# Performance work log

Measured on AMD Instinct MI355X. Metric: run time of the kernel, lower is better.

Reference implementation:

```python
import jax, jax.numpy as jnp
import numpy as np

N = 50000
E = 800000
IN, HID, OUT = 256, 128, 64
NEG_SLOPE = 0.2


def _gat(x, src, dst, W, a_src, a_dst, b, heads, dim, concat):
    # PyG GATConv (eval mode, self-loops already appended to src/dst)
    xh = (x @ W).reshape(N, heads, dim)              # [N,H,D]
    s_src = jnp.einsum('nhd,hd->nh', xh, a_src)       # [N,H]
    s_dst = jnp.einsum('nhd,hd->nh', xh, a_dst)
    e = jax.nn.leaky_relu(s_src[src] + s_dst[dst], NEG_SLOPE)  # [Etot,H]
    m = jax.ops.segment_max(e, dst, num_segments=N)
    e = jnp.exp(e - m[dst])
    z = jax.ops.segment_sum(e, dst, num_segments=N)
    alpha = e / z[dst]                                # segment softmax over incoming edges
    msg = xh[src] * alpha[:, :, None]                 # [Etot,H,D] gather + weight
    out = jax.ops.segment_sum(msg, dst, num_segments=N)  # scatter-add aggregate
    out = out.reshape(N, heads * dim) if concat else out.mean(axis=1)
    return out + b


def setup_inputs():
    key = jax.random.key(0)
    ks = jax.random.split(key, 20)
    sc = 0.05
    inp = {
        'x': jax.random.normal(ks[0], (N, IN), jnp.float32),
        'edge_index': jax.random.randint(ks[1], (2, E), 0, N, jnp.int64) if jax.config.read('jax_enable_x64') else jax.random.randint(ks[1], (2, E), 0, N, jnp.int32),
        # semantic MLP
        'w1': jax.random.normal(ks[2], (IN, HID), jnp.float32) * sc,
        'b1': jnp.zeros((HID,), jnp.float32),
        'w2': jax.random.normal(ks[3], (HID, HID), jnp.float32) * sc,
        'b2': jnp.zeros((HID,), jnp.float32),
        # gat1: HID -> HID//2, heads=4, concat -> 2*HID
        'g1_w': jax.random.normal(ks[4], (HID, 4 * (HID // 2)), jnp.float32) * sc,
        'g1_asrc': jax.random.normal(ks[5], (4, HID // 2), jnp.float32) * sc,
        'g1_adst': jax.random.normal(ks[6], (4, HID // 2), jnp.float32) * sc,
        'g1_b': jnp.zeros((2 * HID,), jnp.float32),
        # gat2: 2*HID -> OUT, heads=2, mean
        'g2_w': jax.random.normal(ks[7], (2 * HID, 2 * OUT), jnp.float32) * sc,
        'g2_asrc': jax.random.normal(ks[8], (2, OUT), jnp.float32) * sc,
        'g2_adst': jax.random.normal(ks[9], (2, OUT), jnp.float32) * sc,
        'g2_b': jnp.zeros((OUT,), jnp.float32),
        # gat3: OUT -> OUT, heads=1, mean
        'g3_w': jax.random.normal(ks[10], (OUT, OUT), jnp.float32) * sc,
        'g3_asrc': jax.random.normal(ks[11], (1, OUT), jnp.float32) * sc,
        'g3_adst': jax.random.normal(ks[12], (1, OUT), jnp.float32) * sc,
        'g3_b': jnp.zeros((OUT,), jnp.float32),
    }
    return inp


def reference(x, edge_index, w1, b1, w2, b2,
              g1_w, g1_asrc, g1_adst, g1_b,
              g2_w, g2_asrc, g2_adst, g2_b,
              g3_w, g3_asrc, g3_adst, g3_b):
    # add self loops once (PyG GATConv default add_self_loops=True)
    loop = jnp.arange(N, dtype=edge_index.dtype)
    src = jnp.concatenate([edge_index[0], loop])
    dst = jnp.concatenate([edge_index[1], loop])
    # semantic MLP (eval: dropout is identity)
    h = jax.nn.relu(x @ w1 + b1)
    h = jax.nn.relu(h @ w2 + b2)
    h = jax.nn.elu(_gat(h, src, dst, g1_w, g1_asrc, g1_adst, g1_b, 4, HID // 2, True))
    h = jax.nn.elu(_gat(h, src, dst, g2_w, g2_asrc, g2_adst, g2_b, 2, OUT, False))
    h = _gat(h, src, dst, g3_w, g3_asrc, g3_adst, g3_b, 1, OUT, False)
    return h
```

## Files before the change

kernel.cpp:

```cpp
#include <hip/hip_runtime.h>
#include <hip/hip_fp16.h>
#include <math.h>

#define NN 50000
#define NE 800000

static inline int ceil_div_h(int a, int b) { return (a + b - 1) / b; }

typedef _Float16 half8 __attribute__((ext_vector_type(8)));
typedef float f32x4 __attribute__((ext_vector_type(4)));

__global__ __launch_bounds__(256)
void prep_kernel(const float* __restrict__ w1, const float* __restrict__ w2,
                 const float* __restrict__ g1w, const float* __restrict__ g2w,
                 const float* __restrict__ g3w, __half* __restrict__ wt,
                 int* __restrict__ cursor) {
  int idx = blockIdx.x * 256 + threadIdx.x;
  if (idx < NN) cursor[idx] = 0;
  const float* W; int K, N, li;
  if (idx < 32768)        { W = w1;  K = 256; N = 128; li = idx; }
  else if (idx < 49152)   { W = w2;  K = 128; N = 128; li = idx - 32768; }
  else if (idx < 81920)   { W = g1w; K = 128; N = 256; li = idx - 49152; }
  else if (idx < 114688)  { W = g2w; K = 256; N = 128; li = idx - 81920; }
  else if (idx < 118784)  { W = g3w; K = 64;  N = 64;  li = idx - 114688; }
  else return;
  int n = li / K, k = li - n * K;
  wt[idx] = __float2half_rn(W[(size_t)k * N + n]);
}

__global__ __launch_bounds__(256)
void mlp_gat1_fused(const float* __restrict__ x,
                    const __half* __restrict__ wt1,
                    const float* __restrict__ b1,
                    const __half* __restrict__ wt2,
                    const float* __restrict__ b2,
                    const __half* __restrict__ wtg1,
                    const float* __restrict__ a_src, const float* __restrict__ a_dst,
                    __half* __restrict__ xh1,
                    float* __restrict__ s_src, float* __restrict__ s_dst) {
  constexpr int SA = 40;
  constexpr int SH = 136;
  __shared__ __align__(16) _Float16 smem[25088];
  _Float16* As   = smem;
  _Float16* Bs12 = smem + 2560;
  _Float16* h1s  = smem + 7680;
  _Float16* h2s  = smem + 16384;
  _Float16* Bs3  = Bs12;
  const int tid = threadIdx.x;
  const int bm = blockIdx.x * 64;
  const int wave = tid >> 6, lane = tid & 63;
  const int l16 = lane & 15, quad = lane >> 4;
  const int wm = (wave & 1) * 32;
  const int wn = (wave >> 1) * 64;

  {
    f32x4 acc[2][4] = {};
    for (int k0 = 0; k0 < 256; k0 += 32) {
      #pragma unroll
      for (int i = 0; i < 2; ++i) {
        int idx = tid + i * 256;
        int m = idx >> 3, q = idx & 7;
        int gm = bm + m;
        float4 v = make_float4(0.f, 0.f, 0.f, 0.f);
        if (gm < NN) v = *(const float4*)&x[(size_t)gm * 256 + k0 + q * 4];
        union { __half2 h2[2]; float2 f2; } u;
        u.h2[0] = __floats2half2_rn(v.x, v.y);
        u.h2[1] = __floats2half2_rn(v.z, v.w);
        *(float2*)&As[m * SA + q * 4] = u.f2;
      }
      #pragma unroll
      for (int i = 0; i < 2; ++i) {
        int idx = tid + i * 256;
        int n = idx >> 2, kq = (idx & 3) * 8;
        *(float4*)&Bs12[n * SA + kq] = *(const float4*)&wt1[(size_t)n * 256 + k0 + kq];
      }
      __syncthreads();
      half8 af[2], bf[4];
      #pragma unroll
      for (int mi = 0; mi < 2; ++mi)
        af[mi] = *(const half8*)&As[(wm + mi * 16 + l16) * SA + quad * 8];
      #pragma unroll
      for (int ni = 0; ni < 4; ++ni)
        bf[ni] = *(const half8*)&Bs12[(wn + ni * 16 + l16) * SA + quad * 8];
      #pragma unroll
      for (int mi = 0; mi < 2; ++mi)
        #pragma unroll
        for (int ni = 0; ni < 4; ++ni)
          acc[mi][ni] = __builtin_amdgcn_mfma_f32_16x16x32_f16(af[mi], bf[ni], acc[mi][ni], 0, 0, 0);
      __syncthreads();
    }
    #pragma unroll
    for (int mi = 0; mi < 2; ++mi)
      #pragma unroll
      for (int r = 0; r < 4; ++r) {
        int row = wm + mi * 16 + quad * 4 + r;
        #pragma unroll
        for (int ni = 0; ni < 4; ++ni) {
          int col = wn + ni * 16 + l16;
          float v = acc[mi][ni][r] + b1[col];
          v = fmaxf(v, 0.f);
          h1s[row * SH + col] = (_Float16)v;
        }
      }
  }
  __syncthreads();

  {
    f32x4 acc[2][4] = {};
    for (int k0 = 0; k0 < 128; k0 += 32) {
      #pragma unroll
      for (int i = 0; i < 2; ++i) {
        int idx = tid + i * 256;
        int n = idx >> 2, kq = (idx & 3) * 8;
        *(float4*)&Bs12[n * SA + kq] = *(const float4*)&wt2[(size_t)n * 128 + k0 + kq];
      }
      __syncthreads();
      half8 af[2], bf[4];
      #pragma unroll
      for (int mi = 0; mi < 2; ++mi)
        af[mi] = *(const half8*)&h1s[(wm + mi * 16 + l16) * SH + k0 + quad * 8];
      #pragma unroll
      for (int ni = 0; ni < 4; ++ni)
        bf[ni] = *(const half8*)&Bs12[(wn + ni * 16 + l16) * SA + quad * 8];
      #pragma unroll
      for (int mi = 0; mi < 2; ++mi)
        #pragma unroll
        for (int ni = 0; ni < 4; ++ni)
          acc[mi][ni] = __builtin_amdgcn_mfma_f32_16x16x32_f16(af[mi], bf[ni], acc[mi][ni], 0, 0, 0);
      __syncthreads();
    }
    #pragma unroll
    for (int mi = 0; mi < 2; ++mi)
      #pragma unroll
      for (int r = 0; r < 4; ++r) {
        int row = wm + mi * 16 + quad * 4 + r;
        #pragma unroll
        for (int ni = 0; ni < 4; ++ni) {
          int col = wn + ni * 16 + l16;
          float v = acc[mi][ni][r] + b2[col];
          v = fmaxf(v, 0.f);
          h2s[row * SH + col] = (_Float16)v;
        }
      }
  }
  __syncthreads();

  {
    f32x4 acc[4][4] = {};
    const int wn3 = wave * 64;
    for (int k0 = 0; k0 < 128; k0 += 32) {
      #pragma unroll
      for (int i = 0; i < 4; ++i) {
        int idx = tid + i * 256;
        int n = idx >> 2, kq = (idx & 3) * 8;
        *(float4*)&Bs3[n * SA + kq] = *(const float4*)&wtg1[(size_t)n * 128 + k0 + kq];
      }
      __syncthreads();
      half8 af[4], bf[4];
      #pragma unroll
      for (int mi = 0; mi < 4; ++mi)
        af[mi] = *(const half8*)&h2s[(mi * 16 + l16) * SH + k0 + quad * 8];
      #pragma unroll
      for (int ni = 0; ni < 4; ++ni)
        bf[ni] = *(const half8*)&Bs3[(wn3 + ni * 16 + l16) * SA + quad * 8];
      #pragma unroll
      for (int mi = 0; mi < 4; ++mi)
        #pragma unroll
        for (int ni = 0; ni < 4; ++ni)
          acc[mi][ni] = __builtin_amdgcn_mfma_f32_16x16x32_f16(af[mi], bf[ni], acc[mi][ni], 0, 0, 0);
      __syncthreads();
    }
    float asv[4], adv[4];
    #pragma unroll
    for (int ni = 0; ni < 4; ++ni) {
      int d = ni * 16 + l16;
      asv[ni] = a_src[wave * 64 + d];
      adv[ni] = a_dst[wave * 64 + d];
    }
    #pragma unroll
    for (int mi = 0; mi < 4; ++mi) {
      #pragma unroll
      for (int r = 0; r < 4; ++r) {
        int gm = bm + mi * 16 + quad * 4 + r;
        float ss = 0.f, sd = 0.f;
        #pragma unroll
        for (int ni = 0; ni < 4; ++ni) {
          float v = acc[mi][ni][r];
          ss = fmaf(v, asv[ni], ss);
          sd = fmaf(v, adv[ni], sd);
          if (gm < NN) xh1[(size_t)gm * 256 + wn3 + ni * 16 + l16] = __float2half_rn(v);
        }
        #pragma unroll
        for (int off = 1; off < 16; off <<= 1) {
          ss += __shfl_xor(ss, off, 64);
          sd += __shfl_xor(sd, off, 64);
        }
        if (l16 == 0 && gm < NN) {
          s_src[gm * 4 + wave] = ss;
          s_dst[gm * 4 + wave] = sd;
        }
      }
    }
  }
}

template<int BM, int TN, int WR, int WC, int ACT, int OUTH, int AF32, int HS>
__global__ __launch_bounds__(256)
void mfma_gemm(const void* __restrict__ Av, const __half* __restrict__ Bt,
               const float* __restrict__ bias, void* __restrict__ Cv,
               const float* __restrict__ a_src, const float* __restrict__ a_dst,
               float* __restrict__ s_src, float* __restrict__ s_dst,
               int M, int N, int K) {
  constexpr int FM = BM / WR / 16;
  constexpr int FN = TN / WC / 16;
  constexpr int SA = 40;
  __shared__ __align__(16) _Float16 As[BM * SA];
  __shared__ __align__(16) _Float16 Bs[TN * SA];
  const int tid = threadIdx.x;
  const int bm = blockIdx.y * BM, bn = blockIdx.x * TN;
  const int wave = tid >> 6, lane = tid & 63;
  const int wm = (wave % WR) * (BM / WR);
  const int wn = (wave / WR) * (TN / WC);
  const int l16 = lane & 15, quad = lane >> 4;

  f32x4 acc[FM][FN] = {};

  for (int k0 = 0; k0 < K; k0 += 32) {
    if (AF32) {
      const float* A = (const float*)Av;
      #pragma unroll
      for (int i = 0; i < (BM * 8) / 256; ++i) {
        int idx = tid + i * 256;
        int m = idx >> 3, q = idx & 7;
        int gm = bm + m;
        float4 v = make_float4(0.f, 0.f, 0.f, 0.f);
        if (gm < M) v = *(const float4*)&A[(size_t)gm * K + k0 + q * 4];
        union { __half2 h2[2]; float2 f2; } u;
        u.h2[0] = __floats2half2_rn(v.x, v.y);
        u.h2[1] = __floats2half2_rn(v.z, v.w);
        *(float2*)&As[m * SA + q * 4] = u.f2;
      }
    } else {
      const __half* A = (const __half*)Av;
      #pragma unroll
      for (int i = 0; i < (BM * 4) / 256; ++i) {
        int idx = tid + i * 256;
        int m = idx >> 2, q = (idx & 3) * 8;
        int gm = bm + m;
        float4 raw = make_float4(0.f, 0.f, 0.f, 0.f);
        if (gm < M) raw = *(const float4*)&A[(size_t)gm * K + k0 + q];
        *(float4*)&As[m * SA + q] = raw;
      }
    }
    #pragma unroll
    for (int i = 0; i < (TN * 4) / 256; ++i) {
      int idx = tid + i * 256;
      int n = idx >> 2, kq = (idx & 3) * 8;
      float4 raw = *(const float4*)&Bt[(size_t)(bn + n) * K + k0 + kq];
      *(float4*)&Bs[n * SA + kq] = raw;
    }
    __syncthreads();
    half8 af[FM], bf[FN];
    #pragma unroll
    for (int mi = 0; mi < FM; ++mi)
      af[mi] = *(const half8*)&As[(wm + mi * 16 + l16) * SA + quad * 8];
    #pragma unroll
    for (int ni = 0; ni < FN; ++ni)
      bf[ni] = *(const half8*)&Bs[(wn + ni * 16 + l16) * SA + quad * 8];
    #pragma unroll
    for (int mi = 0; mi < FM; ++mi)
      #pragma unroll
      for (int ni = 0; ni < FN; ++ni)
        acc[mi][ni] = __builtin_amdgcn_mfma_f32_16x16x32_f16(af[mi], bf[ni], acc[mi][ni], 0, 0, 0);
    __syncthreads();
  }

  #pragma unroll
  for (int mi = 0; mi < FM; ++mi) {
    #pragma unroll
    for (int r = 0; r < 4; ++r) {
      int gm = bm + wm + mi * 16 + quad * 4 + r;
      if (gm >= M) continue;
      #pragma unroll
      for (int ni = 0; ni < FN; ++ni) {
        int gn = bn + wn + ni * 16 + l16;
        float v = acc[mi][ni][r];
        if (bias) v += bias[gn];
        if (ACT == 1) v = fmaxf(v, 0.f);
        if (OUTH) ((__half*)Cv)[(size_t)gm * N + gn] = __float2half_rn(v);
        else      ((float*)Cv)[(size_t)gm * N + gn] = v;
      }
    }
  }

  if (HS > 0) {
    const int h = (bn + wn) >> 6;
    float asv[FN], adv[FN];
    #pragma unroll
    for (int ni = 0; ni < FN; ++ni) {
      int d = ni * 16 + l16;
      asv[ni] = a_src[h * 64 + d];
      adv[ni] = a_dst[h * 64 + d];
    }
    #pragma unroll
    for (int mi = 0; mi < FM; ++mi) {
      #pragma unroll
      for (int r = 0; r < 4; ++r) {
        float ss = 0.f, sd = 0.f;
        #pragma unroll
        for (int ni = 0; ni < FN; ++ni) {
          float v = acc[mi][ni][r];
          ss = fmaf(v, asv[ni], ss);
          sd = fmaf(v, adv[ni], sd);
        }
        #pragma unroll
        for (int off = 1; off < 16; off <<= 1) {
          ss += __shfl_xor(ss, off, 64);
          sd += __shfl_xor(sd, off, 64);
        }
        int gm = bm + wm + mi * 16 + quad * 4 + r;
        if (l16 == 0 && gm < M) {
          s_src[gm * HS + h] = ss;
          s_dst[gm * HS + h] = sd;
        }
      }
    }
  }
}


__global__ __launch_bounds__(256)
void hist_kernel(const int* __restrict__ ei, int* __restrict__ cnt) {
  int e = blockIdx.x * blockDim.x + threadIdx.x;
  if (e >= NE) return;
  atomicAdd(&cnt[ei[NE + e]], 1);
}

__global__ __launch_bounds__(256)
void scan1_kernel(const int* __restrict__ in, int* __restrict__ out,
                  int* __restrict__ bsum, int n) {
  __shared__ int tmp[256];
  int t = threadIdx.x;
  int i = blockIdx.x * 256 + t;
  int v = (i < n) ? in[i] : 0;
  tmp[t] = v;
  __syncthreads();
  for (int off = 1; off < 256; off <<= 1) {
    int u = (t >= off) ? tmp[t - off] : 0;
    __syncthreads();
    tmp[t] += u;
    __syncthreads();
  }
  if (i <= n) out[i] = tmp[t] - v;
  if (t == 255) bsum[blockIdx.x] = tmp[255];
}

__global__ __launch_bounds__(256)
void scan3_kernel(int* __restrict__ out, const int* __restrict__ bsum,
                  int* __restrict__ cursor, int n, int nb) {
  __shared__ int tmp[256];
  int t = threadIdx.x;
  int bv = (t < nb) ? bsum[t] : 0;
  tmp[t] = bv;
  __syncthreads();
  for (int off = 1; off < 256; off <<= 1) {
    int u = (t >= off) ? tmp[t - off] : 0;
    __syncthreads();
    tmp[t] += u;
    __syncthreads();
  }
  int add = tmp[blockIdx.x] - ((blockIdx.x < nb) ? bsum[blockIdx.x] : 0);
  int i = blockIdx.x * 256 + t;
  if (i > n) return;
  int v = out[i] + add;
  out[i] = v;
  if (i < n) cursor[i] = v;
}

__global__ __launch_bounds__(256)
void scatter_kernel(const int* __restrict__ ei, int* __restrict__ cursor,
                    int* __restrict__ srcs) {
  int e = blockIdx.x * blockDim.x + threadIdx.x;
  if (e >= NE) return;
  int s = ei[e], d = ei[NE + e];
  int pos = atomicAdd(&cursor[d], 1);
  srcs[pos] = s;
}

__global__ __launch_bounds__(256)
void gat_aggregate4(const int* __restrict__ rowptr, const int* __restrict__ srcs,
                    const float* __restrict__ ssrc, const float* __restrict__ sdst,
                    const __half* __restrict__ xh, const float* __restrict__ bias,
                    __half* __restrict__ out) {
  constexpr int H = 4, HD = 256;
  __shared__ float wbuf[4][64 * H];
  __shared__ int sbuf[4][64];
  const int wslot = threadIdx.x >> 6;
  const int wid = (blockIdx.x * blockDim.x + threadIdx.x) >> 6;
  const int lane = threadIdx.x & 63;
  if (wid >= NN) return;
  const int n = wid;
  const int start = rowptr[n];
  const int end = rowptr[n + 1];
  const int h = lane >> 4;

  float sdv[H];
  #pragma unroll
  for (int hh = 0; hh < H; ++hh) sdv[hh] = sdst[n * H + hh];

  float z;
  float acc[H];
  {
    float wself[H];
    #pragma unroll
    for (int hh = 0; hh < H; ++hh) {
      float e = ssrc[n * H + hh] + sdv[hh];
      e = e >= 0.f ? e : 0.2f * e;
      wself[hh] = __expf(e);
    }
    float ws = wself[h];
    z = ws;
    const __half* xr = xh + (size_t)n * HD + lane * H;
    float2 raw = *(const float2*)xr;
    __half2 p0 = *(__half2*)&raw.x;
    __half2 p1 = *(__half2*)&raw.y;
    float2 f0 = __half22float2(p0), f1 = __half22float2(p1);
    acc[0] = ws * f0.x; acc[1] = ws * f0.y; acc[2] = ws * f1.x; acc[3] = ws * f1.y;
  }

  for (int base = start; base < end; base += 64) {
    int cnt = end - base;
    if (cnt > 64) cnt = 64;
    if (lane < cnt) {
      int s = srcs[base + lane];
      sbuf[wslot][lane] = s;
      float4 t = *(const float4*)&ssrc[s * 4];
      float ev[H] = {t.x, t.y, t.z, t.w};
      #pragma unroll
      for (int hh = 0; hh < H; ++hh) {
        float e = ev[hh] + sdv[hh];
        e = e >= 0.f ? e : 0.2f * e;
        wbuf[wslot][lane * H + hh] = __expf(e);
      }
    }
    #pragma unroll 4
    for (int j = 0; j < cnt; ++j) {
      int s = sbuf[wslot][j];
      float w = wbuf[wslot][j * H + h];
      z += w;
      const __half* xr = xh + (size_t)s * HD + lane * H;
      float2 raw = *(const float2*)xr;
      __half2 p0 = *(__half2*)&raw.x;
      __half2 p1 = *(__half2*)&raw.y;
      float2 f0 = __half22float2(p0), f1 = __half22float2(p1);
      acc[0] = fmaf(w, f0.x, acc[0]); acc[1] = fmaf(w, f0.y, acc[1]);
      acc[2] = fmaf(w, f1.x, acc[2]); acc[3] = fmaf(w, f1.y, acc[3]);
    }
  }
  const float inv = 1.f / z;

  float v[4];
  #pragma unroll
  for (int i = 0; i < 4; ++i) {
    v[i] = acc[i] * inv + bias[lane * 4 + i];
    v[i] = v[i] > 0.f ? v[i] : expm1f(v[i]);
  }
  union { __half2 h2[2]; float2 f2; } u;
  u.h2[0] = __floats2half2_rn(v[0], v[1]);
  u.h2[1] = __floats2half2_rn(v[2], v[3]);
  *(float2*)&out[(size_t)n * 256 + lane * 4] = u.f2;
}

template<int H, int MODE>
__global__ __launch_bounds__(256)
void gat_aggregate_sub(const int* __restrict__ rowptr, const int* __restrict__ srcs,
                       const float* __restrict__ ssrc, const float* __restrict__ sdst,
                       const __half* __restrict__ xh, const float* __restrict__ bias,
                       void* __restrict__ outv) {
  constexpr int HD   = H * 64;
  constexpr int GL   = HD / 4;
  constexpr int NSUB = 64 / GL;
  const int wid  = (blockIdx.x * blockDim.x + threadIdx.x) >> 6;
  const int lane = threadIdx.x & 63;
  const int sg = lane / GL;
  const int p  = lane - sg * GL;
  const int n  = wid * NSUB + sg;
  const int hp = (p * 4) >> 6;
  const bool alive = (n < NN);

  int start = 0, end = 0;
  float sdv = 0.f;
  if (alive) {
    start = rowptr[n];
    end = rowptr[n + 1];
    sdv = sdst[n * H + hp];
  }

  float z = 0.f;
  float a0 = 0.f, a1 = 0.f, a2 = 0.f, a3 = 0.f;

  if (alive) {
    float e = ssrc[n * H + hp] + sdv;
    e = e >= 0.f ? e : 0.2f * e;
    float w = __expf(e);
    z = w;
    float2 raw = *(const float2*)(xh + (size_t)n * HD + p * 4);
    __half2 p0 = *(__half2*)&raw.x, p1 = *(__half2*)&raw.y;
    float2 f0 = __half22float2(p0), f1 = __half22float2(p1);
    a0 = w * f0.x; a1 = w * f0.y; a2 = w * f1.x; a3 = w * f1.y;
  }

  for (int j = start; j < end; ++j) {
    int s = srcs[j];
    float e = ssrc[s * H + hp] + sdv;
    e = e >= 0.f ? e : 0.2f * e;
    float w = __expf(e);
    z += w;
    float2 raw = *(const float2*)(xh + (size_t)s * HD + p * 4);
    __half2 p0 = *(__half2*)&raw.x, p1 = *(__half2*)&raw.y;
    float2 f0 = __half22float2(p0), f1 = __half22float2(p1);
    a0 = fmaf(w, f0.x, a0); a1 = fmaf(w, f0.y, a1);
    a2 = fmaf(w, f1.x, a2); a3 = fmaf(w, f1.y, a3);
  }

  const float inv = 1.f / z;

  if (MODE == 1) {
    float v0 = a0 * inv, v1 = a1 * inv, v2 = a2 * inv, v3 = a3 * inv;
    float o0 = __shfl_xor(v0, 16, 64);
    float o1 = __shfl_xor(v1, 16, 64);
    float o2 = __shfl_xor(v2, 16, 64);
    float o3 = __shfl_xor(v3, 16, 64);
    if (alive && hp == 0) {
      float m0 = (v0 + o0) * 0.5f + bias[p * 4 + 0];
      float m1 = (v1 + o1) * 0.5f + bias[p * 4 + 1];
      float m2 = (v2 + o2) * 0.5f + bias[p * 4 + 2];
      float m3 = (v3 + o3) * 0.5f + bias[p * 4 + 3];
      m0 = m0 > 0.f ? m0 : expm1f(m0);
      m1 = m1 > 0.f ? m1 : expm1f(m1);
      m2 = m2 > 0.f ? m2 : expm1f(m2);
      m3 = m3 > 0.f ? m3 : expm1f(m3);
      __half* out = (__half*)outv;
      union { __half2 h2[2]; float2 f2; } u;
      u.h2[0] = __floats2half2_rn(m0, m1);
      u.h2[1] = __floats2half2_rn(m2, m3);
      *(float2*)&out[(size_t)n * 64 + p * 4] = u.f2;
    }
  } else {
    if (alive) {
      float* out = (float*)outv;
      float4 o = make_float4(a0 * inv + bias[p * 4 + 0],
                             a1 * inv + bias[p * 4 + 1],
                             a2 * inv + bias[p * 4 + 2],
                             a3 * inv + bias[p * 4 + 3]);
      *(float4*)&out[(size_t)n * 64 + p * 4] = o;
    }
  }
}


extern "C" void kernel_launch(void* const* d_in, const int* in_sizes, int n_in,
                              void* d_out, int out_size, void* d_ws, size_t ws_size,
                              hipStream_t stream) {
  const float* x    = (const float*)d_in[0];
  const int*   ei   = (const int*)d_in[1];
  const float* w1   = (const float*)d_in[2];
  const float* b1   = (const float*)d_in[3];
  const float* w2   = (const float*)d_in[4];
  const float* b2   = (const float*)d_in[5];
  const float* g1w  = (const float*)d_in[6];
  const float* g1as = (const float*)d_in[7];
  const float* g1ad = (const float*)d_in[8];
  const float* g1b  = (const float*)d_in[9];
  const float* g2w  = (const float*)d_in[10];
  const float* g2as = (const float*)d_in[11];
  const float* g2ad = (const float*)d_in[12];
  const float* g2b  = (const float*)d_in[13];
  const float* g3w  = (const float*)d_in[14];
  const float* g3as = (const float*)d_in[15];
  const float* g3ad = (const float*)d_in[16];
  const float* g3b  = (const float*)d_in[17];
  float* out = (float*)d_out;

  float* ws   = (float*)d_ws;
  float* bufA = ws;
  float* bufB = bufA + (size_t)NN * 256;
  float* bufC = bufB + (size_t)NN * 256;
  float* ssrc = bufC + (size_t)NN * 256;
  float* sdst = ssrc + (size_t)NN * 4;
  int* rowptr = (int*)(sdst + (size_t)NN * 4);
  int* cursor = rowptr + (NN + 1);
  int* bsum   = cursor + NN;
  int* srcs   = bsum + 256;
  __half* wt   = (__half*)(srcs + NE);
  __half* wt1  = wt;
  __half* wt2  = wt + 32768;
  __half* wtg1 = wt + 49152;
  __half* wtg2 = wt + 81920;
  __half* wtg3 = wt + 114688;

  __half* xh1 = (__half*)bufC;
  __half* a1  = (__half*)bufA;
  __half* xh2 = (__half*)bufB;
  __half* a2  = (__half*)bufC;
  __half* xh3 = (__half*)bufB;

  const int TB = 256;
  const int grid_m = ceil_div_h(NN, 64);
  const int egrid = ceil_div_h(NE, TB);
  const int sgrid = ceil_div_h(NN + 1, TB);
  const int wgrid = ceil_div_h(NN, 4);

  prep_kernel<<<ceil_div_h(118784, TB), TB, 0, stream>>>(w1, w2, g1w, g2w, g3w, wt, cursor);

  hist_kernel<<<egrid, TB, 0, stream>>>(ei, cursor);
  scan1_kernel<<<sgrid, TB, 0, stream>>>(cursor, rowptr, bsum, NN);
  scan3_kernel<<<sgrid, TB, 0, stream>>>(rowptr, bsum, cursor, NN, sgrid);
  scatter_kernel<<<egrid, TB, 0, stream>>>(ei, cursor, srcs);

  mlp_gat1_fused<<<grid_m, TB, 0, stream>>>(x, wt1, b1, wt2, b2, wtg1,
                                            g1as, g1ad, xh1, ssrc, sdst);
  gat_aggregate4<<<wgrid, TB, 0, stream>>>(rowptr, srcs, ssrc, sdst, xh1, g1b, a1);

  mfma_gemm<64, 128, 2, 2, 0, 1, 0, 2><<<dim3(1, grid_m), TB, 0, stream>>>(
      a1, wtg2, nullptr, xh2, g2as, g2ad, ssrc, sdst, NN, 128, 256);
  gat_aggregate_sub<2, 1><<<ceil_div_h(NN, 8), TB, 0, stream>>>(
      rowptr, srcs, ssrc, sdst, xh2, g2b, a2);

  mfma_gemm<64, 64, 4, 1, 0, 1, 0, 1><<<dim3(1, grid_m), TB, 0, stream>>>(
      a2, wtg3, nullptr, xh3, g3as, g3ad, ssrc, sdst, NN, 64, 64);
  gat_aggregate_sub<1, 2><<<ceil_div_h(NN, 16), TB, 0, stream>>>(
      rowptr, srcs, ssrc, sdst, xh3, g3b, out);
}
```

Measured before the change: 431.0 us.

## Aggregate GAT layers 2/3 with one wavefront per node and edge sub-groups

Replaces the sub-wavefront-per-node aggregation for the second and third GAT layers with one wavefront per destination node. Lanes are split into sub-groups that process different incoming edges in parallel, and the partial sums are combined with xor shuffles at the end. Each 64-edge chunk has its attention weights and source indices computed once and staged in shared memory, so the exp is not recomputed per lane. This gives more memory-level parallelism per node, at the cost of launching more wavefronts and leaving lanes idle on low-degree nodes.

```diff
diff --git a/kernel.cpp b/kernel.cpp
--- a/kernel.cpp
+++ b/kernel.cpp
@@ -473,56 +473,92 @@
 
 template<int H, int MODE>
 __global__ __launch_bounds__(256)
-void gat_aggregate_sub(const int* __restrict__ rowptr, const int* __restrict__ srcs,
-                       const float* __restrict__ ssrc, const float* __restrict__ sdst,
-                       const __half* __restrict__ xh, const float* __restrict__ bias,
-                       void* __restrict__ outv) {
+void gat_aggregate_ms(const int* __restrict__ rowptr, const int* __restrict__ srcs,
+                      const float* __restrict__ ssrc, const float* __restrict__ sdst,
+                      const __half* __restrict__ xh, const float* __restrict__ bias,
+                      void* __restrict__ outv) {
   constexpr int HD   = H * 64;
-  constexpr int GL   = HD / 4;
-  constexpr int NSUB = 64 / GL;
-  const int wid  = (blockIdx.x * blockDim.x + threadIdx.x) >> 6;
+  constexpr int L8   = HD / 4;
+  constexpr int NSUB = 64 / L8;
+  __shared__ float wbuf[4][64 * H];
+  __shared__ int sbuf[4][64];
+  const int wslot = threadIdx.x >> 6;
+  const int wid = (blockIdx.x * blockDim.x + threadIdx.x) >> 6;
   const int lane = threadIdx.x & 63;
-  const int sg = lane / GL;
-  const int p  = lane - sg * GL;
-  const int n  = wid * NSUB + sg;
+  if (wid >= NN) return;
+  const int n = wid;
+  const int start = rowptr[n];
+  const int end = rowptr[n + 1];
+  const int sub = lane / L8;
+  const int p = lane - sub * L8;
   const int hp = (p * 4) >> 6;
-  const bool alive = (n < NN);
-
-  int start = 0, end = 0;
-  float sdv = 0.f;
-  if (alive) {
-    start = rowptr[n];
-    end = rowptr[n + 1];
-    sdv = sdst[n * H + hp];
-  }
+
+  float sdv[H];
+  #pragma unroll
+  for (int hh = 0; hh < H; ++hh) sdv[hh] = sdst[n * H + hh];
 
   float z = 0.f;
   float a0 = 0.f, a1 = 0.f, a2 = 0.f, a3 = 0.f;
-
-  if (alive) {
-    float e = ssrc[n * H + hp] + sdv;
+  {
+    float e = ssrc[n * H + hp] + sdv[hp];
     e = e >= 0.f ? e : 0.2f * e;
-    float w = __expf(e);
-    z = w;
-    float2 raw = *(const float2*)(xh + (size_t)n * HD + p * 4);
-    __half2 p0 = *(__half2*)&raw.x, p1 = *(__half2*)&raw.y;
-    float2 f0 = __half22float2(p0), f1 = __half22float2(p1);
-    a0 = w * f0.x; a1 = w * f0.y; a2 = w * f1.x; a3 = w * f1.y;
-  }
-
-  for (int j = start; j < end; ++j) {
-    int s = srcs[j];
-    float e = ssrc[s * H + hp] + sdv;
-    e = e >= 0.f ? e : 0.2f * e;
-    float w = __expf(e);
-    z += w;
-    float2 raw = *(const float2*)(xh + (size_t)s * HD + p * 4);
-    __half2 p0 = *(__half2*)&raw.x, p1 = *(__half2*)&raw.y;
-    float2 f0 = __half22float2(p0), f1 = __half22float2(p1);
-    a0 = fmaf(w, f0.x, a0); a1 = fmaf(w, f0.y, a1);
-    a2 = fmaf(w, f1.x, a2); a3 = fmaf(w, f1.y, a3);
-  }
-
+    float ws = __expf(e);
+    if (sub == 0) {
+      z = ws;
+      float2 raw = *(const float2*)(xh + (size_t)n * HD + p * 4);
+      __half2 q0 = *(__half2*)&raw.x, q1 = *(__half2*)&raw.y;
+      float2 f0 = __half22float2(q0), f1 = __half22float2(q1);
+      a0 = ws * f0.x; a1 = ws * f0.y; a2 = ws * f1.x; a3 = ws * f1.y;
+    }
+  }
+
+  for (int base = start; base < end; base += 64) {
+    int cnt = end - base;
+    if (cnt > 64) cnt = 64;
+    int cnt_pad = (cnt + NSUB - 1) & ~(NSUB - 1);
+    if (lane < cnt) {
+      int s = srcs[base + lane];
+      sbuf[wslot][lane] = s;
+      float ev[H];
+      if (H == 2) {
+        float2 t = *(const float2*)&ssrc[s * 2];
+        ev[0] = t.x; ev[1] = t.y;
+      } else {
+        ev[0] = ssrc[s];
+      }
+      #pragma unroll
+      for (int hh = 0; hh < H; ++hh) {
+        float e = ev[hh] + sdv[hh];
+        e = e >= 0.f ? e : 0.2f * e;
+        wbuf[wslot][lane * H + hh] = __expf(e);
+      }
+    } else if (lane < cnt_pad) {
+      sbuf[wslot][lane] = n;
+      #pragma unroll
+      for (int hh = 0; hh < H; ++hh) wbuf[wslot][lane * H + hh] = 0.f;
+    }
+    #pragma unroll 4
+    for (int j = 0; j < cnt; j += NSUB) {
+      int e = j + sub;
+      int s = sbuf[wslot][e];
+      float w = wbuf[wslot][e * H + hp];
+      z += w;
+      float2 raw = *(const float2*)(xh + (size_t)s * HD + p * 4);
+      __half2 q0 = *(__half2*)&raw.x, q1 = *(__half2*)&raw.y;
+      float2 f0 = __half22float2(q0), f1 = __half22float2(q1);
+      a0 = fmaf(w, f0.x, a0); a1 = fmaf(w, f0.y, a1);
+      a2 = fmaf(w, f1.x, a2); a3 = fmaf(w, f1.y, a3);
+    }
+  }
+
+  #pragma unroll
+  for (int m = L8; m < 64; m <<= 1) {
+    z += __shfl_xor(z, m, 64);
+    a0 += __shfl_xor(a0, m, 64);
+    a1 += __shfl_xor(a1, m, 64);
+    a2 += __shfl_xor(a2, m, 64);
+    a3 += __shfl_xor(a3, m, 64);
+  }
   const float inv = 1.f / z;
 
   if (MODE == 1) {
@@ -531,7 +567,7 @@
     float o1 = __shfl_xor(v1, 16, 64);
     float o2 = __shfl_xor(v2, 16, 64);
     float o3 = __shfl_xor(v3, 16, 64);
-    if (alive && hp == 0) {
+    if (sub == 0 && hp == 0) {
       float m0 = (v0 + o0) * 0.5f + bias[p * 4 + 0];
       float m1 = (v1 + o1) * 0.5f + bias[p * 4 + 1];
       float m2 = (v2 + o2) * 0.5f + bias[p * 4 + 2];
@@ -547,7 +583,7 @@
       *(float2*)&out[(size_t)n * 64 + p * 4] = u.f2;
     }
   } else {
-    if (alive) {
+    if (sub == 0) {
       float* out = (float*)outv;
       float4 o = make_float4(a0 * inv + bias[p * 4 + 0],
                              a1 * inv + bias[p * 4 + 1],
@@ -624,11 +660,11 @@
 
   mfma_gemm<64, 128, 2, 2, 0, 1, 0, 2><<<dim3(1, grid_m), TB, 0, stream>>>(
       a1, wtg2, nullptr, xh2, g2as, g2ad, ssrc, sdst, NN, 128, 256);
-  gat_aggregate_sub<2, 1><<<ceil_div_h(NN, 8), TB, 0, stream>>>(
+  gat_aggregate_ms<2, 1><<<wgrid, TB, 0, stream>>>(
       rowptr, srcs, ssrc, sdst, xh2, g2b, a2);
 
   mfma_gemm<64, 64, 4, 1, 0, 1, 0, 1><<<dim3(1, grid_m), TB, 0, stream>>>(
       a2, wtg3, nullptr, xh3, g3as, g3ad, ssrc, sdst, NN, 64, 64);
-  gat_aggregate_sub<1, 2><<<ceil_div_h(NN, 16), TB, 0, stream>>>(
+  gat_aggregate_ms<1, 2><<<wgrid, TB, 0, stream>>>(
       rowptr, srcs, ssrc, sdst, xh3, g3b, out);
 }
```

After: 396.5 us. 8.0% less time.
